# Kernel tuning notes

Measured on AMD Instinct MI355X. Metric: run time of the kernel, lower is better.

Reference implementation:

```python
import jax, jax.numpy as jnp
import numpy as np

N_USERS = 100000
N_ITEMS = 50000
N_NODES = N_USERS + N_ITEMS
EMB = 64
N_LAYERS = 3
N_EDGES = 4800000
AVG_DEG = 32


def setup_inputs() -> dict:
    key = jax.random.key(0)
    k1, k2, k3, k4, k5 = jax.random.split(key, 5)
    user_emb = jax.random.normal(k1, (N_USERS, EMB), dtype=jnp.float32) * 0.01
    item_emb = jax.random.normal(k2, (N_ITEMS, EMB), dtype=jnp.float32) * 0.01
    # normalized adjacency values ~ 1/deg
    adj_val = jax.random.uniform(k3, (N_EDGES,), dtype=jnp.float32) * (1.0 / AVG_DEG)
    adj_row = jax.random.randint(k4, (N_EDGES,), 0, N_NODES, dtype=jnp.int32)
    adj_col = jax.random.randint(k5, (N_EDGES,), 0, N_NODES, dtype=jnp.int32)
    return {"user_emb": user_emb, "item_emb": item_emb,
            "adj_val": adj_val, "adj_row": adj_row, "adj_col": adj_col}


def reference(user_emb, item_emb, adj_val, adj_row, adj_col):
    ego = jnp.concatenate([user_emb, item_emb], axis=0)  # [N_NODES, EMB]

    def spmm(x):
        # sparse_adj @ x via gather + segment-sum over destination rows
        msgs = adj_val[:, None] * x[adj_col]              # [N_EDGES, EMB]
        return jax.ops.segment_sum(msgs, adj_row, num_segments=N_NODES)

    acc = ego  # running sum for layer-mean (avoids stacking all layers)
    x = ego
    for _ in range(N_LAYERS):
        x = jax.nn.relu(spmm(x))
        acc = acc + x
    all_emb = acc / (N_LAYERS + 1)
    return all_emb[:N_USERS], all_emb[N_USERS:]
```

## Files before the change

kernel.cpp:

```cpp
#include <hip/hip_runtime.h>

#define N_USERS 100000
#define N_ITEMS 50000
#define N_NODES 150000
#define EMB 64
#define N_EDGES 4800000
#define N_LAYERS 3

#define RPB 128
#define NB 1172
#define MAXB 5120
#define CHUNK 8192
#define NCHUNKS ((N_EDGES + CHUNK - 1) / CHUNK)

__global__ __launch_bounds__(256) void init_kernel(
        const float2* __restrict__ user, const float2* __restrict__ item,
        unsigned short* __restrict__ x8, float* __restrict__ xs,
        float2* __restrict__ out) {
    int t = threadIdx.x;
    int p = t & 31;
    int r = blockIdx.x * 8 + (t >> 5);
    if (r >= N_NODES) return;
    float2 e = (r < N_USERS) ? user[r * 32 + p] : item[(r - N_USERS) * 32 + p];
    int o = r * 32 + p;
    out[o] = make_float2(0.25f * e.x, 0.25f * e.y);
    float m = fmaxf(fabsf(e.x), fabsf(e.y));
    #pragma unroll
    for (int mask = 16; mask; mask >>= 1) m = fmaxf(m, __shfl_xor(m, mask));
    float inv = (m > 0.f) ? 127.0f / m : 0.f;
    int q0 = (int)rintf(e.x * inv) + 128;
    int q1 = (int)rintf(e.y * inv) + 128;
    x8[o] = (unsigned short)(q0 | (q1 << 8));
    if (p == 0) xs[r] = m * (1.0f / 127.0f);
}

__global__ __launch_bounds__(256) void hist_kernel(
        const int* __restrict__ row, int* __restrict__ counts) {
    __shared__ int h[NB];
    for (int i = threadIdx.x; i < NB; i += 256) h[i] = 0;
    __syncthreads();
    for (int i = blockIdx.x * 256 + threadIdx.x; i < N_EDGES; i += gridDim.x * 256)
        atomicAdd(&h[row[i] >> 7], 1);
    __syncthreads();
    for (int i = threadIdx.x; i < NB; i += 256) {
        int v = h[i];
        if (v) atomicAdd(&counts[i], v);
    }
}

__global__ __launch_bounds__(1024) void scan_kernel(
        const int* __restrict__ counts,
        int* __restrict__ bucketStart, int* __restrict__ cursor) {
    __shared__ int tmp[1024];
    int t = threadIdx.x;
    int i0 = 2 * t, i1 = 2 * t + 1;
    int v0 = (i0 < NB) ? counts[i0] : 0;
    int v1 = (i1 < NB) ? counts[i1] : 0;
    int s = v0 + v1;
    tmp[t] = s;
    __syncthreads();
    for (int off = 1; off < 1024; off <<= 1) {
        int u = (t >= off) ? tmp[t - off] : 0;
        __syncthreads();
        tmp[t] += u;
        __syncthreads();
    }
    int excl = tmp[t] - s;
    if (i0 < NB) { bucketStart[i0] = excl;      cursor[i0] = excl; }
    if (i1 < NB) { bucketStart[i1] = excl + v0; cursor[i1] = excl + v0; }
    if (t == 0) bucketStart[NB] = N_EDGES;
}

__global__ __launch_bounds__(512) void chunkscatter_kernel(
        const int* __restrict__ row, const int* __restrict__ col,
        const float* __restrict__ val,
        int* __restrict__ cursor, int2* __restrict__ sEdge) {
    __shared__ int2 rec[CHUNK];
    __shared__ unsigned short bidS[CHUNK];
    __shared__ int cnt[NB];
    __shared__ int lofs[NB];
    __shared__ int gbase[NB];
    __shared__ int tmp[512];

    int t = threadIdx.x;
    int e0 = blockIdx.x * CHUNK;
    int n = N_EDGES - e0; if (n > CHUNK) n = CHUNK;

    for (int i = t; i < NB; i += 512) cnt[i] = 0;
    __syncthreads();

    int2 myrec[16];
    int  myb[16];
    #pragma unroll
    for (int j = 0; j < 16; ++j) {
        int i = j * 512 + t;
        if (i < n) {
            int gi = e0 + i;
            int r = row[gi];
            int b = r >> 7;
            myrec[j] = make_int2(((r & (RPB - 1)) << 18) | col[gi],
                                 __float_as_int(val[gi]));
            myb[j] = b;
            atomicAdd(&cnt[b], 1);
        } else myb[j] = -1;
    }
    __syncthreads();

    int b3 = t * 3;
    int c0 = (b3     < NB) ? cnt[b3]     : 0;
    int c1 = (b3 + 1 < NB) ? cnt[b3 + 1] : 0;
    int c2 = (b3 + 2 < NB) ? cnt[b3 + 2] : 0;
    int s = c0 + c1 + c2;
    tmp[t] = s;
    __syncthreads();
    for (int off = 1; off < 512; off <<= 1) {
        int u = (t >= off) ? tmp[t - off] : 0;
        __syncthreads();
        tmp[t] += u;
        __syncthreads();
    }
    int excl = tmp[t] - s;
    if (b3     < NB) lofs[b3]     = excl;
    if (b3 + 1 < NB) lofs[b3 + 1] = excl + c0;
    if (b3 + 2 < NB) lofs[b3 + 2] = excl + c0 + c1;
    __syncthreads();

    for (int i = t; i < NB; i += 512) {
        int c = cnt[i];
        gbase[i] = c ? atomicAdd(&cursor[i], c) : 0;
        cnt[i] = lofs[i];
    }
    __syncthreads();

    #pragma unroll
    for (int j = 0; j < 16; ++j) {
        if (myb[j] >= 0) {
            int p = atomicAdd(&cnt[myb[j]], 1);
            rec[p] = myrec[j];
            bidS[p] = (unsigned short)myb[j];
        }
    }
    __syncthreads();

    for (int i = t; i < n; i += 512) {
        int b = bidS[i];
        sEdge[gbase[b] + (i - lofs[b])] = rec[i];
    }
}

__global__ __launch_bounds__(256) void localsort_kernel(
        const int* __restrict__ bucketStart, int2* __restrict__ sEdge,
        int* __restrict__ rowStart) {
    __shared__ int2 sorted[MAXB];
    __shared__ int lh[RPB];
    __shared__ int lsc[RPB];
    __shared__ int lcur[RPB];
    int b = blockIdx.x, t = threadIdx.x;
    int s0 = bucketStart[b];
    int s1 = bucketStart[b + 1];
    int size = s1 - s0;

    int2 e[20];
    #pragma unroll
    for (int j = 0; j < 20; ++j) {
        int idx = s0 + j * 256 + t;
        if (idx < s1) e[j] = sEdge[idx];
    }
    if (t < RPB) lh[t] = 0;
    __syncthreads();
    #pragma unroll
    for (int j = 0; j < 20; ++j) {
        int idx = s0 + j * 256 + t;
        if (idx < s1) atomicAdd(&lh[e[j].x >> 18], 1);
    }
    __syncthreads();
    if (t < RPB) lsc[t] = lh[t];
    __syncthreads();
    for (int off = 1; off < RPB; off <<= 1) {
        int u = 0;
        if (t < RPB && t >= off) u = lsc[t - off];
        __syncthreads();
        if (t < RPB) lsc[t] += u;
        __syncthreads();
    }
    if (t < RPB) {
        int excl = lsc[t] - lh[t];
        lcur[t] = excl;
        int node = b * RPB + t;
        if (node <= N_NODES) rowStart[node] = s0 + excl;
    }
    __syncthreads();
    #pragma unroll
    for (int j = 0; j < 20; ++j) {
        int idx = s0 + j * 256 + t;
        if (idx < s1) {
            int rl = e[j].x >> 18;
            int pos = atomicAdd(&lcur[rl], 1);
            sorted[pos] = make_int2((e[j].x & 0x3FFFF) << 6, e[j].y);
        }
    }
    __syncthreads();
    for (int j = t; j < size; j += 256) sEdge[s0 + j] = sorted[j];
}

template<int BIASED>
__global__ __launch_bounds__(256, 4) void gather_kernel(
        const int* __restrict__ rowStart, const int2* __restrict__ sEdge,
        const unsigned short* __restrict__ x8, const float* __restrict__ xs,
        unsigned short* __restrict__ y8, float* __restrict__ ys,
        float2* __restrict__ out, int last) {
    __shared__ int2 eds[8][32];
    int t = threadIdx.x;
    int p = t & 31;
    int h = t >> 5;
    int r = blockIdx.x * 8 + h;
    if (r >= N_NODES) return;
    int start = rowStart[r];
    int end   = rowStart[r + 1];
    float2 acc = make_float2(0.f, 0.f);
    float ws = 0.f;
    const char* __restrict__ xp = (const char*)x8 + 2 * p;

    for (int base = start; base < end; base += 32) {
        int idx = base + p;
        int2 ed = (idx < end) ? sEdge[idx] : make_int2(0, 0);
        float w0 = __int_as_float(ed.y) * xs[ed.x >> 6];
        eds[h][p] = make_int2(ed.x, __float_as_int(w0));

        int cnt = end - base; if (cnt > 32) cnt = 32;
        int nb = (cnt + 7) >> 3;
        for (int s8 = 0; s8 < nb; ++s8) {
            #pragma unroll
            for (int jj = 0; jj < 8; ++jj) {
                int2 e = eds[h][s8 * 8 + jj];
                float w = __int_as_float(e.y);
                unsigned q = *(const unsigned short*)(xp + e.x);
                acc.x = fmaf(w, (float)(q & 0xFFu), acc.x);
                acc.y = fmaf(w, (float)((q >> 8) & 0xFFu), acc.y);
                if (BIASED) ws += w;
            }
        }
    }
    if (BIASED) {
        acc.x = fmaf(-128.f, ws, acc.x);
        acc.y = fmaf(-128.f, ws, acc.y);
    }

    float rx = fmaxf(acc.x, 0.f);
    float ry = fmaxf(acc.y, 0.f);
    int o = r * 32 + p;
    float2 ov = out[o];
    ov.x += 0.25f * rx; ov.y += 0.25f * ry;
    out[o] = ov;
    if (!last) {
        float m = fmaxf(rx, ry);
        #pragma unroll
        for (int mask = 16; mask; mask >>= 1) m = fmaxf(m, __shfl_xor(m, mask));
        float inv = (m > 0.f) ? 255.0f / m : 0.f;
        int q0 = (int)(rx * inv + 0.5f);
        int q1 = (int)(ry * inv + 0.5f);
        y8[o] = (unsigned short)(q0 | (q1 << 8));
        if (p == 0) ys[r] = m * (1.0f / 255.0f);
    }
}

extern "C" void kernel_launch(void* const* d_in, const int* in_sizes, int n_in,
                              void* d_out, int out_size, void* d_ws, size_t ws_size,
                              hipStream_t stream) {
    const float* user_emb = (const float*)d_in[0];
    const float* item_emb = (const float*)d_in[1];
    const float* adj_val  = (const float*)d_in[2];
    const int*   adj_row  = (const int*)d_in[3];
    const int*   adj_col  = (const int*)d_in[4];
    float* out = (float*)d_out;

    char* p = (char*)d_ws;
    int*  counts      = (int*)p;  p += ((size_t)NB * 4 + 15) & ~15ull;
    int*  bucketStart = (int*)p;  p += ((size_t)(NB + 1) * 4 + 15) & ~15ull;
    int*  cursor      = (int*)p;  p += ((size_t)NB * 4 + 15) & ~15ull;
    int*  rowStart    = (int*)p;  p += ((size_t)(N_NODES + 1) * 4 + 15) & ~15ull;
    int2* sEdge       = (int2*)p; p += (size_t)N_EDGES * 8;
    unsigned short* xq0 = (unsigned short*)p; p += (size_t)N_NODES * EMB;
    unsigned short* xq1 = (unsigned short*)p; p += (size_t)N_NODES * EMB;
    float* xsc0       = (float*)p; p += (size_t)N_NODES * 4;
    float* xsc1       = (float*)p;

    const int rowBlocks = (N_NODES + 7) / 8;

    init_kernel<<<rowBlocks, 256, 0, stream>>>(
        (const float2*)user_emb, (const float2*)item_emb,
        xq0, xsc0, (float2*)out);

    hipMemsetAsync(counts, 0, (size_t)NB * 4, stream);
    hist_kernel<<<512, 256, 0, stream>>>(adj_row, counts);
    scan_kernel<<<1, 1024, 0, stream>>>(counts, bucketStart, cursor);
    chunkscatter_kernel<<<NCHUNKS, 512, 0, stream>>>(
        adj_row, adj_col, adj_val, cursor, sEdge);
    localsort_kernel<<<NB, 256, 0, stream>>>(bucketStart, sEdge, rowStart);

    unsigned short* x = xq0; float* sx = xsc0;
    unsigned short* y = xq1; float* sy = xsc1;
    for (int l = 0; l < N_LAYERS; ++l) {
        if (l == 0)
            gather_kernel<1><<<rowBlocks, 256, 0, stream>>>(
                rowStart, sEdge, x, sx, y, sy, (float2*)out, 0);
        else
            gather_kernel<0><<<rowBlocks, 256, 0, stream>>>(
                rowStart, sEdge, x, sx, y, sy, (float2*)out, l == N_LAYERS - 1);
        unsigned short* tq = x; x = y; y = tq;
        float* ts = sx; sx = sy; sy = ts;
    }
}
```

Before: 567.9 us.

## Replace bucketed two-pass CSR sort with per-row atomic counting scatter

Result: slower. 914.0 us (+61.0%).

```diff
diff --git a/kernel.cpp b/kernel.cpp
--- a/kernel.cpp
+++ b/kernel.cpp
@@ -7,205 +7,75 @@
 #define N_EDGES 4800000
 #define N_LAYERS 3
 
-#define RPB 128
-#define NB 1172
-#define MAXB 5120
-#define CHUNK 8192
-#define NCHUNKS ((N_EDGES + CHUNK - 1) / CHUNK)
+#define INIT_BLOCKS 18750
+#define HIST_BLOCKS 512
 
-__global__ __launch_bounds__(256) void init_kernel(
+__global__ __launch_bounds__(256) void inithist_kernel(
         const float2* __restrict__ user, const float2* __restrict__ item,
         unsigned short* __restrict__ x8, float* __restrict__ xs,
-        float2* __restrict__ out) {
+        float2* __restrict__ out,
+        const int* __restrict__ row, int* __restrict__ deg) {
     int t = threadIdx.x;
-    int p = t & 31;
-    int r = blockIdx.x * 8 + (t >> 5);
-    if (r >= N_NODES) return;
-    float2 e = (r < N_USERS) ? user[r * 32 + p] : item[(r - N_USERS) * 32 + p];
-    int o = r * 32 + p;
-    out[o] = make_float2(0.25f * e.x, 0.25f * e.y);
-    float m = fmaxf(fabsf(e.x), fabsf(e.y));
-    #pragma unroll
-    for (int mask = 16; mask; mask >>= 1) m = fmaxf(m, __shfl_xor(m, mask));
-    float inv = (m > 0.f) ? 127.0f / m : 0.f;
-    int q0 = (int)rintf(e.x * inv) + 128;
-    int q1 = (int)rintf(e.y * inv) + 128;
-    x8[o] = (unsigned short)(q0 | (q1 << 8));
-    if (p == 0) xs[r] = m * (1.0f / 127.0f);
-}
-
-__global__ __launch_bounds__(256) void hist_kernel(
-        const int* __restrict__ row, int* __restrict__ counts) {
-    __shared__ int h[NB];
-    for (int i = threadIdx.x; i < NB; i += 256) h[i] = 0;
-    __syncthreads();
-    for (int i = blockIdx.x * 256 + threadIdx.x; i < N_EDGES; i += gridDim.x * 256)
-        atomicAdd(&h[row[i] >> 7], 1);
-    __syncthreads();
-    for (int i = threadIdx.x; i < NB; i += 256) {
-        int v = h[i];
-        if (v) atomicAdd(&counts[i], v);
+    if (blockIdx.x < INIT_BLOCKS) {
+        int p = t & 31;
+        int r = blockIdx.x * 8 + (t >> 5);
+        if (r >= N_NODES) return;
+        float2 e = (r < N_USERS) ? user[r * 32 + p] : item[(r - N_USERS) * 32 + p];
+        int o = r * 32 + p;
+        out[o] = make_float2(0.25f * e.x, 0.25f * e.y);
+        float m = fmaxf(fabsf(e.x), fabsf(e.y));
+        #pragma unroll
+        for (int mask = 16; mask; mask >>= 1) m = fmaxf(m, __shfl_xor(m, mask));
+        float inv = (m > 0.f) ? 127.0f / m : 0.f;
+        int q0 = (int)rintf(e.x * inv) + 128;
+        int q1 = (int)rintf(e.y * inv) + 128;
+        x8[o] = (unsigned short)(q0 | (q1 << 8));
+        if (p == 0) xs[r] = m * (1.0f / 127.0f);
+    } else {
+        int bh = blockIdx.x - INIT_BLOCKS;
+        for (int i = bh * 256 + t; i < N_EDGES; i += HIST_BLOCKS * 256)
+            atomicAdd(&deg[row[i]], 1);
     }
 }
 
-__global__ __launch_bounds__(1024) void scan_kernel(
-        const int* __restrict__ counts,
-        int* __restrict__ bucketStart, int* __restrict__ cursor) {
-    __shared__ int tmp[1024];
-    int t = threadIdx.x;
-    int i0 = 2 * t, i1 = 2 * t + 1;
-    int v0 = (i0 < NB) ? counts[i0] : 0;
-    int v1 = (i1 < NB) ? counts[i1] : 0;
-    int s = v0 + v1;
-    tmp[t] = s;
-    __syncthreads();
-    for (int off = 1; off < 1024; off <<= 1) {
-        int u = (t >= off) ? tmp[t - off] : 0;
-        __syncthreads();
-        tmp[t] += u;
-        __syncthreads();
+__global__ __launch_bounds__(256) void alloc_kernel(
+        const int* __restrict__ deg, int* __restrict__ startArr,
+        int* __restrict__ cur, int* __restrict__ gc) {
+    int r = blockIdx.x * 256 + threadIdx.x;
+    int lane = threadIdx.x & 63;
+    int d = (r < N_NODES) ? deg[r] : 0;
+    int pre = d;
+    #pragma unroll
+    for (int off = 1; off < 64; off <<= 1) {
+        int u = __shfl_up(pre, off);
+        if (lane >= off) pre += u;
     }
-    int excl = tmp[t] - s;
-    if (i0 < NB) { bucketStart[i0] = excl;      cursor[i0] = excl; }
-    if (i1 < NB) { bucketStart[i1] = excl + v0; cursor[i1] = excl + v0; }
-    if (t == 0) bucketStart[NB] = N_EDGES;
-}
-
-__global__ __launch_bounds__(512) void chunkscatter_kernel(
-        const int* __restrict__ row, const int* __restrict__ col,
-        const float* __restrict__ val,
-        int* __restrict__ cursor, int2* __restrict__ sEdge) {
-    __shared__ int2 rec[CHUNK];
-    __shared__ unsigned short bidS[CHUNK];
-    __shared__ int cnt[NB];
-    __shared__ int lofs[NB];
-    __shared__ int gbase[NB];
-    __shared__ int tmp[512];
-
-    int t = threadIdx.x;
-    int e0 = blockIdx.x * CHUNK;
-    int n = N_EDGES - e0; if (n > CHUNK) n = CHUNK;
-
-    for (int i = t; i < NB; i += 512) cnt[i] = 0;
-    __syncthreads();
-
-    int2 myrec[16];
-    int  myb[16];
-    #pragma unroll
-    for (int j = 0; j < 16; ++j) {
-        int i = j * 512 + t;
-        if (i < n) {
-            int gi = e0 + i;
-            int r = row[gi];
-            int b = r >> 7;
-            myrec[j] = make_int2(((r & (RPB - 1)) << 18) | col[gi],
-                                 __float_as_int(val[gi]));
-            myb[j] = b;
-            atomicAdd(&cnt[b], 1);
-        } else myb[j] = -1;
-    }
-    __syncthreads();
-
-    int b3 = t * 3;
-    int c0 = (b3     < NB) ? cnt[b3]     : 0;
-    int c1 = (b3 + 1 < NB) ? cnt[b3 + 1] : 0;
-    int c2 = (b3 + 2 < NB) ? cnt[b3 + 2] : 0;
-    int s = c0 + c1 + c2;
-    tmp[t] = s;
-    __syncthreads();
-    for (int off = 1; off < 512; off <<= 1) {
-        int u = (t >= off) ? tmp[t - off] : 0;
-        __syncthreads();
-        tmp[t] += u;
-        __syncthreads();
-    }
-    int excl = tmp[t] - s;
-    if (b3     < NB) lofs[b3]     = excl;
-    if (b3 + 1 < NB) lofs[b3 + 1] = excl + c0;
-    if (b3 + 2 < NB) lofs[b3 + 2] = excl + c0 + c1;
-    __syncthreads();
-
-    for (int i = t; i < NB; i += 512) {
-        int c = cnt[i];
-        gbase[i] = c ? atomicAdd(&cursor[i], c) : 0;
-        cnt[i] = lofs[i];
-    }
-    __syncthreads();
-
-    #pragma unroll
-    for (int j = 0; j < 16; ++j) {
-        if (myb[j] >= 0) {
-            int p = atomicAdd(&cnt[myb[j]], 1);
-            rec[p] = myrec[j];
-            bidS[p] = (unsigned short)myb[j];
-        }
-    }
-    __syncthreads();
-
-    for (int i = t; i < n; i += 512) {
-        int b = bidS[i];
-        sEdge[gbase[b] + (i - lofs[b])] = rec[i];
+    int tot = __shfl(pre, 63);
+    int excl = pre - d;
+    int base = 0;
+    if (lane == 63) base = atomicAdd(gc, tot);
+    base = __shfl(base, 63);
+    if (r < N_NODES) {
+        startArr[r] = base + excl;
+        cur[r]      = base + excl;
     }
 }
 
-__global__ __launch_bounds__(256) void localsort_kernel(
-        const int* __restrict__ bucketStart, int2* __restrict__ sEdge,
-        int* __restrict__ rowStart) {
-    __shared__ int2 sorted[MAXB];
-    __shared__ int lh[RPB];
-    __shared__ int lsc[RPB];
-    __shared__ int lcur[RPB];
-    int b = blockIdx.x, t = threadIdx.x;
-    int s0 = bucketStart[b];
-    int s1 = bucketStart[b + 1];
-    int size = s1 - s0;
-
-    int2 e[20];
-    #pragma unroll
-    for (int j = 0; j < 20; ++j) {
-        int idx = s0 + j * 256 + t;
-        if (idx < s1) e[j] = sEdge[idx];
-    }
-    if (t < RPB) lh[t] = 0;
-    __syncthreads();
-    #pragma unroll
-    for (int j = 0; j < 20; ++j) {
-        int idx = s0 + j * 256 + t;
-        if (idx < s1) atomicAdd(&lh[e[j].x >> 18], 1);
-    }
-    __syncthreads();
-    if (t < RPB) lsc[t] = lh[t];
-    __syncthreads();
-    for (int off = 1; off < RPB; off <<= 1) {
-        int u = 0;
-        if (t < RPB && t >= off) u = lsc[t - off];
-        __syncthreads();
-        if (t < RPB) lsc[t] += u;
-        __syncthreads();
-    }
-    if (t < RPB) {
-        int excl = lsc[t] - lh[t];
-        lcur[t] = excl;
-        int node = b * RPB + t;
-        if (node <= N_NODES) rowStart[node] = s0 + excl;
-    }
-    __syncthreads();
-    #pragma unroll
-    for (int j = 0; j < 20; ++j) {
-        int idx = s0 + j * 256 + t;
-        if (idx < s1) {
-            int rl = e[j].x >> 18;
-            int pos = atomicAdd(&lcur[rl], 1);
-            sorted[pos] = make_int2((e[j].x & 0x3FFFF) << 6, e[j].y);
-        }
-    }
-    __syncthreads();
-    for (int j = t; j < size; j += 256) sEdge[s0 + j] = sorted[j];
+__global__ __launch_bounds__(256) void scatter_kernel(
+        const int* __restrict__ row, const int* __restrict__ col,
+        const float* __restrict__ val,
+        int* __restrict__ cur, int2* __restrict__ sEdge) {
+    int i = blockIdx.x * 256 + threadIdx.x;
+    if (i >= N_EDGES) return;
+    int r = row[i];
+    int pos = atomicAdd(&cur[r], 1);
+    sEdge[pos] = make_int2(col[i] << 6, __float_as_int(val[i]));
 }
 
 template<int BIASED>
 __global__ __launch_bounds__(256, 4) void gather_kernel(
-        const int* __restrict__ rowStart, const int2* __restrict__ sEdge,
+        const int* __restrict__ startArr, const int* __restrict__ deg,
+        const int2* __restrict__ sEdge,
         const unsigned short* __restrict__ x8, const float* __restrict__ xs,
         unsigned short* __restrict__ y8, float* __restrict__ ys,
         float2* __restrict__ out, int last) {
@@ -215,8 +85,8 @@
     int h = t >> 5;
     int r = blockIdx.x * 8 + h;
     if (r >= N_NODES) return;
-    int start = rowStart[r];
-    int end   = rowStart[r + 1];
+    int start = startArr[r];
+    int end   = start + deg[r];
     float2 acc = make_float2(0.f, 0.f);
     float ws = 0.f;
     const char* __restrict__ xp = (const char*)x8 + 2 * p;
@@ -275,38 +145,38 @@
     float* out = (float*)d_out;
 
     char* p = (char*)d_ws;
-    int*  counts      = (int*)p;  p += ((size_t)NB * 4 + 15) & ~15ull;
-    int*  bucketStart = (int*)p;  p += ((size_t)(NB + 1) * 4 + 15) & ~15ull;
-    int*  cursor      = (int*)p;  p += ((size_t)NB * 4 + 15) & ~15ull;
-    int*  rowStart    = (int*)p;  p += ((size_t)(N_NODES + 1) * 4 + 15) & ~15ull;
-    int2* sEdge       = (int2*)p; p += (size_t)N_EDGES * 8;
+    int*  deg      = (int*)p;  p += ((size_t)N_NODES * 4 + 15) & ~15ull;
+    int*  gc       = (int*)p;  p += 16;
+    int*  startArr = (int*)p;  p += ((size_t)N_NODES * 4 + 15) & ~15ull;
+    int*  cur      = (int*)p;  p += ((size_t)N_NODES * 4 + 15) & ~15ull;
+    int2* sEdge    = (int2*)p; p += (size_t)N_EDGES * 8;
     unsigned short* xq0 = (unsigned short*)p; p += (size_t)N_NODES * EMB;
     unsigned short* xq1 = (unsigned short*)p; p += (size_t)N_NODES * EMB;
-    float* xsc0       = (float*)p; p += (size_t)N_NODES * 4;
-    float* xsc1       = (float*)p;
+    float* xsc0    = (float*)p; p += (size_t)N_NODES * 4;
+    float* xsc1    = (float*)p;
+
+    hipMemsetAsync(deg, 0, ((size_t)N_NODES * 4 + 15 & ~15ull) + 16, stream);
+
+    inithist_kernel<<<INIT_BLOCKS + HIST_BLOCKS, 256, 0, stream>>>(
+        (const float2*)user_emb, (const float2*)item_emb,
+        xq0, xsc0, (float2*)out, adj_row, deg);
+
+    alloc_kernel<<<(N_NODES + 255) / 256, 256, 0, stream>>>(
+        deg, startArr, cur, gc);
+
+    scatter_kernel<<<(N_EDGES + 255) / 256, 256, 0, stream>>>(
+        adj_row, adj_col, adj_val, cur, sEdge);
 
     const int rowBlocks = (N_NODES + 7) / 8;
-
-    init_kernel<<<rowBlocks, 256, 0, stream>>>(
-        (const float2*)user_emb, (const float2*)item_emb,
-        xq0, xsc0, (float2*)out);
-
-    hipMemsetAsync(counts, 0, (size_t)NB * 4, stream);
-    hist_kernel<<<512, 256, 0, stream>>>(adj_row, counts);
-    scan_kernel<<<1, 1024, 0, stream>>>(counts, bucketStart, cursor);
-    chunkscatter_kernel<<<NCHUNKS, 512, 0, stream>>>(
-        adj_row, adj_col, adj_val, cursor, sEdge);
-    localsort_kernel<<<NB, 256, 0, stream>>>(bucketStart, sEdge, rowStart);
-
     unsigned short* x = xq0; float* sx = xsc0;
     unsigned short* y = xq1; float* sy = xsc1;
     for (int l = 0; l < N_LAYERS; ++l) {
         if (l == 0)
             gather_kernel<1><<<rowBlocks, 256, 0, stream>>>(
-                rowStart, sEdge, x, sx, y, sy, (float2*)out, 0);
+                startArr, deg, sEdge, x, sx, y, sy, (float2*)out, 0);
         else
             gather_kernel<0><<<rowBlocks, 256, 0, stream>>>(
-                rowStart, sEdge, x, sx, y, sy, (float2*)out, l == N_LAYERS - 1);
+                startArr, deg, sEdge, x, sx, y, sy, (float2*)out, l == N_LAYERS - 1);
         unsigned short* tq = x; x = y; y = tq;
         float* ts = sx; sx = sy; sy = ts;
     }
```

## Replace histogram and scan with fixed-capacity buckets for the edge sort

Applied to the files above, without the earlier changes.

New measurement: 538.9 us. -5.1%, faster.

```diff
diff --git a/kernel.cpp b/kernel.cpp
--- a/kernel.cpp
+++ b/kernel.cpp
@@ -9,9 +9,11 @@
 
 #define RPB 128
 #define NB 1172
-#define MAXB 5120
+#define CAP 4608
 #define CHUNK 8192
+#define EPT (CHUNK / 512)
 #define NCHUNKS ((N_EDGES + CHUNK - 1) / CHUNK)
+#define LS_EPT (CAP / 256)
 
 __global__ __launch_bounds__(256) void init_kernel(
         const float2* __restrict__ user, const float2* __restrict__ item,
@@ -34,43 +36,6 @@
     if (p == 0) xs[r] = m * (1.0f / 127.0f);
 }
 
-__global__ __launch_bounds__(256) void hist_kernel(
-        const int* __restrict__ row, int* __restrict__ counts) {
-    __shared__ int h[NB];
-    for (int i = threadIdx.x; i < NB; i += 256) h[i] = 0;
-    __syncthreads();
-    for (int i = blockIdx.x * 256 + threadIdx.x; i < N_EDGES; i += gridDim.x * 256)
-        atomicAdd(&h[row[i] >> 7], 1);
-    __syncthreads();
-    for (int i = threadIdx.x; i < NB; i += 256) {
-        int v = h[i];
-        if (v) atomicAdd(&counts[i], v);
-    }
-}
-
-__global__ __launch_bounds__(1024) void scan_kernel(
-        const int* __restrict__ counts,
-        int* __restrict__ bucketStart, int* __restrict__ cursor) {
-    __shared__ int tmp[1024];
-    int t = threadIdx.x;
-    int i0 = 2 * t, i1 = 2 * t + 1;
-    int v0 = (i0 < NB) ? counts[i0] : 0;
-    int v1 = (i1 < NB) ? counts[i1] : 0;
-    int s = v0 + v1;
-    tmp[t] = s;
-    __syncthreads();
-    for (int off = 1; off < 1024; off <<= 1) {
-        int u = (t >= off) ? tmp[t - off] : 0;
-        __syncthreads();
-        tmp[t] += u;
-        __syncthreads();
-    }
-    int excl = tmp[t] - s;
-    if (i0 < NB) { bucketStart[i0] = excl;      cursor[i0] = excl; }
-    if (i1 < NB) { bucketStart[i1] = excl + v0; cursor[i1] = excl + v0; }
-    if (t == 0) bucketStart[NB] = N_EDGES;
-}
-
 __global__ __launch_bounds__(512) void chunkscatter_kernel(
         const int* __restrict__ row, const int* __restrict__ col,
         const float* __restrict__ val,
@@ -89,10 +54,10 @@
     for (int i = t; i < NB; i += 512) cnt[i] = 0;
     __syncthreads();
 
-    int2 myrec[16];
-    int  myb[16];
-    #pragma unroll
-    for (int j = 0; j < 16; ++j) {
+    int2 myrec[EPT];
+    int  myb[EPT];
+    #pragma unroll
+    for (int j = 0; j < EPT; ++j) {
         int i = j * 512 + t;
         if (i < n) {
             int gi = e0 + i;
@@ -133,7 +98,7 @@
     __syncthreads();
 
     #pragma unroll
-    for (int j = 0; j < 16; ++j) {
+    for (int j = 0; j < EPT; ++j) {
         if (myb[j] >= 0) {
             int p = atomicAdd(&cnt[myb[j]], 1);
             rec[p] = myrec[j];
@@ -144,34 +109,32 @@
 
     for (int i = t; i < n; i += 512) {
         int b = bidS[i];
-        sEdge[gbase[b] + (i - lofs[b])] = rec[i];
-    }
-}
-
-__global__ __launch_bounds__(256) void localsort_kernel(
-        const int* __restrict__ bucketStart, int2* __restrict__ sEdge,
-        int* __restrict__ rowStart) {
-    __shared__ int2 sorted[MAXB];
+        int pos = gbase[b] + (i - lofs[b]);
+        if (pos < CAP) sEdge[b * CAP + pos] = rec[i];
+    }
+}
+
+__global__ __launch_bounds__(256, 4) void localsort_kernel(
+        const int* __restrict__ cursor, int2* __restrict__ sEdge,
+        int* __restrict__ rowStart, int* __restrict__ rowCnt) {
     __shared__ int lh[RPB];
     __shared__ int lsc[RPB];
     __shared__ int lcur[RPB];
     int b = blockIdx.x, t = threadIdx.x;
-    int s0 = bucketStart[b];
-    int s1 = bucketStart[b + 1];
-    int size = s1 - s0;
-
-    int2 e[20];
-    #pragma unroll
-    for (int j = 0; j < 20; ++j) {
-        int idx = s0 + j * 256 + t;
-        if (idx < s1) e[j] = sEdge[idx];
+    int s0 = b * CAP;
+    int size = cursor[b]; if (size > CAP) size = CAP;
+
+    int2 e[LS_EPT];
+    #pragma unroll
+    for (int j = 0; j < LS_EPT; ++j) {
+        int idx = j * 256 + t;
+        if (idx < size) e[j] = sEdge[s0 + idx];
     }
     if (t < RPB) lh[t] = 0;
     __syncthreads();
     #pragma unroll
-    for (int j = 0; j < 20; ++j) {
-        int idx = s0 + j * 256 + t;
-        if (idx < s1) atomicAdd(&lh[e[j].x >> 18], 1);
+    for (int j = 0; j < LS_EPT; ++j) {
+        if (j * 256 + t < size) atomicAdd(&lh[e[j].x >> 18], 1);
     }
     __syncthreads();
     if (t < RPB) lsc[t] = lh[t];
@@ -187,25 +150,26 @@
         int excl = lsc[t] - lh[t];
         lcur[t] = excl;
         int node = b * RPB + t;
-        if (node <= N_NODES) rowStart[node] = s0 + excl;
-    }
-    __syncthreads();
-    #pragma unroll
-    for (int j = 0; j < 20; ++j) {
-        int idx = s0 + j * 256 + t;
-        if (idx < s1) {
+        if (node < N_NODES) {
+            rowStart[node] = s0 + excl;
+            rowCnt[node]   = lh[t];
+        }
+    }
+    __syncthreads();
+    #pragma unroll
+    for (int j = 0; j < LS_EPT; ++j) {
+        if (j * 256 + t < size) {
             int rl = e[j].x >> 18;
             int pos = atomicAdd(&lcur[rl], 1);
-            sorted[pos] = make_int2((e[j].x & 0x3FFFF) << 6, e[j].y);
-        }
-    }
-    __syncthreads();
-    for (int j = t; j < size; j += 256) sEdge[s0 + j] = sorted[j];
+            sEdge[s0 + pos] = make_int2((e[j].x & 0x3FFFF) << 6, e[j].y);
+        }
+    }
 }
 
 template<int BIASED>
 __global__ __launch_bounds__(256, 4) void gather_kernel(
-        const int* __restrict__ rowStart, const int2* __restrict__ sEdge,
+        const int* __restrict__ rowStart, const int* __restrict__ rowCnt,
+        const int2* __restrict__ sEdge,
         const unsigned short* __restrict__ x8, const float* __restrict__ xs,
         unsigned short* __restrict__ y8, float* __restrict__ ys,
         float2* __restrict__ out, int last) {
@@ -216,7 +180,7 @@
     int r = blockIdx.x * 8 + h;
     if (r >= N_NODES) return;
     int start = rowStart[r];
-    int end   = rowStart[r + 1];
+    int end   = start + rowCnt[r];
     float2 acc = make_float2(0.f, 0.f);
     float ws = 0.f;
     const char* __restrict__ xp = (const char*)x8 + 2 * p;
@@ -275,38 +239,36 @@
     float* out = (float*)d_out;
 
     char* p = (char*)d_ws;
-    int*  counts      = (int*)p;  p += ((size_t)NB * 4 + 15) & ~15ull;
-    int*  bucketStart = (int*)p;  p += ((size_t)(NB + 1) * 4 + 15) & ~15ull;
-    int*  cursor      = (int*)p;  p += ((size_t)NB * 4 + 15) & ~15ull;
-    int*  rowStart    = (int*)p;  p += ((size_t)(N_NODES + 1) * 4 + 15) & ~15ull;
-    int2* sEdge       = (int2*)p; p += (size_t)N_EDGES * 8;
+    int*  cursor   = (int*)p;  p += ((size_t)NB * 4 + 15) & ~15ull;
+    int*  rowStart = (int*)p;  p += ((size_t)N_NODES * 4 + 15) & ~15ull;
+    int*  rowCnt   = (int*)p;  p += ((size_t)N_NODES * 4 + 15) & ~15ull;
+    int2* sEdge    = (int2*)p; p += (size_t)NB * CAP * 8;
     unsigned short* xq0 = (unsigned short*)p; p += (size_t)N_NODES * EMB;
     unsigned short* xq1 = (unsigned short*)p; p += (size_t)N_NODES * EMB;
-    float* xsc0       = (float*)p; p += (size_t)N_NODES * 4;
-    float* xsc1       = (float*)p;
-
-    const int rowBlocks = (N_NODES + 7) / 8;
-
-    init_kernel<<<rowBlocks, 256, 0, stream>>>(
+    float* xsc0    = (float*)p; p += (size_t)N_NODES * 4;
+    float* xsc1    = (float*)p;
+
+    hipMemsetAsync(cursor, 0, (size_t)NB * 4, stream);
+
+    init_kernel<<<(N_NODES + 7) / 8, 256, 0, stream>>>(
         (const float2*)user_emb, (const float2*)item_emb,
         xq0, xsc0, (float2*)out);
 
-    hipMemsetAsync(counts, 0, (size_t)NB * 4, stream);
-    hist_kernel<<<512, 256, 0, stream>>>(adj_row, counts);
-    scan_kernel<<<1, 1024, 0, stream>>>(counts, bucketStart, cursor);
     chunkscatter_kernel<<<NCHUNKS, 512, 0, stream>>>(
         adj_row, adj_col, adj_val, cursor, sEdge);
-    localsort_kernel<<<NB, 256, 0, stream>>>(bucketStart, sEdge, rowStart);
-
+
+    localsort_kernel<<<NB, 256, 0, stream>>>(cursor, sEdge, rowStart, rowCnt);
+
+    const int rowBlocks = (N_NODES + 7) / 8;
     unsigned short* x = xq0; float* sx = xsc0;
     unsigned short* y = xq1; float* sy = xsc1;
     for (int l = 0; l < N_LAYERS; ++l) {
         if (l == 0)
             gather_kernel<1><<<rowBlocks, 256, 0, stream>>>(
-                rowStart, sEdge, x, sx, y, sy, (float2*)out, 0);
+                rowStart, rowCnt, sEdge, x, sx, y, sy, (float2*)out, 0);
         else
             gather_kernel<0><<<rowBlocks, 256, 0, stream>>>(
-                rowStart, sEdge, x, sx, y, sy, (float2*)out, l == N_LAYERS - 1);
+                rowStart, rowCnt, sEdge, x, sx, y, sy, (float2*)out, l == N_LAYERS - 1);
         unsigned short* tq = x; x = y; y = tq;
         float* ts = sx; sx = sy; sy = ts;
     }
```
